# Kernel tuning notes

Hardware: AMD Instinct MI355X
Metric: run time of the kernel (lower is better)

Reference implementation:

```python
import jax, jax.numpy as jnp
import numpy as np

B, L, D = 8, 8192, 512
TARGET_RATIO = 1.0 / 6.0


def _normalize(v):
    # matches torch F.normalize(dim=-1, eps=1e-12)
    n = jnp.maximum(jnp.linalg.norm(v, axis=-1, keepdims=True), 1e-12)
    return v / n


def _downsample(x, b_hard):
    # vectorized stream compaction, padded to L (static upper bound of L_max)
    Bb, Ll, Dd = x.shape
    cnt = jnp.cumsum(b_hard.astype(jnp.int32), axis=1)
    pos = jnp.where(b_hard > 0.5, cnt - 1, Ll)          # non-selected -> dump slot L
    bidx = jnp.arange(Bb)[:, None]
    out = jnp.zeros((Bb, Ll + 1, Dd), x.dtype).at[bidx, pos].set(x)[:, :Ll]
    counts = cnt[:, -1]
    mask = jnp.arange(Ll)[None, :] < counts[:, None]
    return out, mask


def setup_inputs() -> dict:
    key = jax.random.key(0)
    k1, k2, k3 = jax.random.split(key, 3)
    x = jax.random.normal(k1, (B, L, D), jnp.float32)
    W_q = jax.random.normal(k2, (D, D), jnp.float32) / np.sqrt(D)
    W_k = jax.random.normal(k3, (D, D), jnp.float32) / np.sqrt(D)
    return {"x": x, "W_q": W_q, "W_k": W_k}


def reference(x, W_q, W_k):
    q = _normalize(jnp.einsum('bld,ed->ble', x, W_q))   # nn.Linear: x @ W.T
    k = _normalize(jnp.einsum('bld,ed->ble', x, W_k))
    k_prev = jnp.pad(k[:, :-1, :], ((0, 0), (1, 0), (0, 0)))
    cos_sim = jnp.sum(q * k_prev, axis=-1)               # (B, L)
    p = jnp.clip(0.5 * (1.0 - cos_sim), 0.0, 1.0)
    p = p.at[:, 0].set(1.0)                              # first position always boundary
    b_hard = (p >= 0.5).astype(x.dtype)
    N = 1.0 / TARGET_RATIO
    F_actual = jnp.mean(b_hard)
    G_actual = jnp.mean(p)
    ratio_loss = N / (N - 1.0) * ((N - 1.0) * F_actual * G_actual + (1.0 - F_actual) * (1.0 - G_actual))
    compressed, comp_mask = _downsample(x, b_hard)
    p_compressed, _ = _downsample(p[..., None], b_hard)
    p_compressed = p_compressed[..., 0]
    return (compressed, comp_mask, b_hard, p, p_compressed, ratio_loss)
```

## Files before the change

### kernel.cpp

```cpp
#include <hip/hip_runtime.h>
#include <hip/hip_bf16.h>
#include <math.h>

#define BB 8
#define LL 8192
#define DD 512
#define NROWS (BB * LL)

#define OUT_COMP   0
#define OUT_MASK   33554432
#define OUT_BHARD  33619968
#define OUT_P      33685504
#define OUT_PCOMP  33751040
#define OUT_LOSS   33816576

#define WS_FIXLIST 0
#define WS_FIXCNT  262144
#define WS_COUNTS  262148
#define WS_SUMP    262180
#define WS_SEL     262212
#define WS_SSK     524416
#define WS_SSQ     786560
#define WS_DOT     1048704
#define WS_WQH     1310848
#define WS_WQL     1835136
#define WS_WKH     2359424
#define WS_WKL     2883712

#define FIX_CAP 65536
#define FIX_TAU 1e-4f

typedef __attribute__((ext_vector_type(8))) _Float16 half8;
typedef __attribute__((ext_vector_type(4))) float f32x4;

static __device__ __forceinline__ void ld_g2l16(const void* g, void* l) {
  __builtin_amdgcn_global_load_lds(
      (const __attribute__((address_space(1))) void*)g,
      (__attribute__((address_space(3))) void*)l, 16, 0, 0);
}

__global__ __launch_bounds__(256) void wsplit(
    const float* __restrict__ Wq, const float* __restrict__ Wk,
    _Float16* __restrict__ wqh, _Float16* __restrict__ wql,
    _Float16* __restrict__ wkh, _Float16* __restrict__ wkl,
    float* __restrict__ ssk, float* __restrict__ ssq,
    float* __restrict__ dotb, int* __restrict__ fixcnt) {
  const int t = blockIdx.x * 256 + threadIdx.x;
  if (t == 0) *fixcnt = 0;
  ssk[t] = 0.0f;
  ssq[t] = 0.0f;
  dotb[t] = 0.0f;

  const int m = t >> 15;
  const int c = t & 32767;
  const int kt = c >> 11;
  const int ct = (c >> 6) & 31;
  const int l = c & 63;
  const int n = l & 15;
  const int kblk = l >> 4;
  const int e = ct * 16 + n;
  const int d0 = kt * 32 + kblk * 8;
  const float* src = (m ? Wk : Wq) + (long)e * 512 + d0;
  _Float16* dh = (m ? wkh : wqh) + (long)c * 8;
  _Float16* dl = (m ? wkl : wql) + (long)c * 8;
  float4 v0 = *(const float4*)src;
  float4 v1 = *(const float4*)(src + 4);
  float av[8] = {v0.x, v0.y, v0.z, v0.w, v1.x, v1.y, v1.z, v1.w};
  half8 hi, lo;
#pragma unroll
  for (int j = 0; j < 8; ++j) {
    _Float16 hh = (_Float16)av[j];
    hi[j] = hh;
    lo[j] = (_Float16)(av[j] - (float)hh);
  }
  *(half8*)dh = hi;
  *(half8*)dl = lo;
}

template <int PASS>
__global__ __launch_bounds__(256, 2) void gemm_tile(
    const float* __restrict__ x, const _Float16* __restrict__ wh,
    const _Float16* __restrict__ wl, _Float16* __restrict__ kbuf,
    float* __restrict__ ssOut, float* __restrict__ dotOut) {
  __shared__ _Float16 smem[16384];
  _Float16* AH = smem;
  _Float16* AL = AH + 4096;
  _Float16* BH = AL + 4096;
  _Float16* BL = BH + 4096;

  const int tid = threadIdx.x;
  const int lane = tid & 63;
  const int w = tid >> 6;
  const int wrow = w & 1, wcol = w >> 1;
  const int g = lane >> 4, n = lane & 15;
  const int bx = blockIdx.x;
  const int rb = bx >> 2, cb = bx & 3;
  const long r0 = (long)rb * 128;

  const int arow = ((tid >> 6) << 4) | (tid & 15);
  const int akb = (tid >> 4) & 3;
  const float* ap = x + (r0 + arow) * 512 + akb * 8;

  f32x4 acc[4][4];
#pragma unroll
  for (int mb = 0; mb < 4; ++mb)
#pragma unroll
    for (int nb = 0; nb < 4; ++nb) acc[mb][nb] = (f32x4){0.f, 0.f, 0.f, 0.f};

  float4 f0 = *(const float4*)(ap);
  float4 f1 = *(const float4*)(ap + 4);
  float4 f2 = *(const float4*)(ap + 64 * 512);
  float4 f3 = *(const float4*)(ap + 64 * 512 + 4);

  for (int kt = 0; kt < 16; ++kt) {
    const long bbase = ((long)(kt * 32 + cb * 8) << 9) + w * 1024 + lane * 8;
    ld_g2l16(wh + bbase, BH + w * 1024);
    ld_g2l16(wh + bbase + 512, BH + w * 1024 + 512);
    ld_g2l16(wl + bbase, BL + w * 1024);
    ld_g2l16(wl + bbase + 512, BL + w * 1024 + 512);
    {
      float av0[8] = {f0.x, f0.y, f0.z, f0.w, f1.x, f1.y, f1.z, f1.w};
      float av1[8] = {f2.x, f2.y, f2.z, f2.w, f3.x, f3.y, f3.z, f3.w};
      half8 h0, h1, l0, l1;
#pragma unroll
      for (int j = 0; j < 8; ++j) {
        _Float16 a = (_Float16)av0[j];
        h0[j] = a;
        l0[j] = (_Float16)(av0[j] - (float)a);
        _Float16 b = (_Float16)av1[j];
        h1[j] = b;
        l1[j] = (_Float16)(av1[j] - (float)b);
      }
      *(half8*)(AH + tid * 8) = h0;
      *(half8*)(AH + (tid + 256) * 8) = h1;
      *(half8*)(AL + tid * 8) = l0;
      *(half8*)(AL + (tid + 256) * 8) = l1;
    }
    __syncthreads();
    if (kt < 15) {
      const float* xp = ap + (kt + 1) * 32;
      f0 = *(const float4*)(xp);
      f1 = *(const float4*)(xp + 4);
      f2 = *(const float4*)(xp + 64 * 512);
      f3 = *(const float4*)(xp + 64 * 512 + 4);
    }
    half8 ah[4], al[4], bh[4], bl[4];
#pragma unroll
    for (int mb = 0; mb < 4; ++mb) {
      const int cm = wrow * 4 + mb;
      ah[mb] = *(const half8*)(AH + (cm * 64 + lane) * 8);
      al[mb] = *(const half8*)(AL + (cm * 64 + lane) * 8);
    }
#pragma unroll
    for (int nb = 0; nb < 4; ++nb) {
      bh[nb] = *(const half8*)(BH + ((wcol * 4 + nb) * 64 + lane) * 8);
      bl[nb] = *(const half8*)(BL + ((wcol * 4 + nb) * 64 + lane) * 8);
    }
#pragma unroll
    for (int nb = 0; nb < 4; ++nb)
#pragma unroll
      for (int mb = 0; mb < 4; ++mb) {
        acc[mb][nb] = __builtin_amdgcn_mfma_f32_16x16x32_f16(ah[mb], bh[nb], acc[mb][nb], 0, 0, 0);
        acc[mb][nb] = __builtin_amdgcn_mfma_f32_16x16x32_f16(al[mb], bh[nb], acc[mb][nb], 0, 0, 0);
        acc[mb][nb] = __builtin_amdgcn_mfma_f32_16x16x32_f16(ah[mb], bl[nb], acc[mb][nb], 0, 0, 0);
      }
    __syncthreads();
  }

  const int colbase = cb * 128 + wcol * 64 + n;
#pragma unroll
  for (int mb = 0; mb < 4; ++mb) {
#pragma unroll
    for (int reg = 0; reg < 4; ++reg) {
      const long row = r0 + wrow * 64 + mb * 16 + g * 4 + reg;
      float ss = 0.f, dt = 0.f;
      const long rp = (row > 0) ? row - 1 : 0;
#pragma unroll
      for (int nb = 0; nb < 4; ++nb) {
        float v = acc[mb][nb][reg];
        ss = fmaf(v, v, ss);
        if (PASS == 1) {
          kbuf[row * 512 + colbase + nb * 16] = (_Float16)v;
        } else {
          float kp = (float)kbuf[rp * 512 + colbase + nb * 16];
          dt = fmaf(v, kp, dt);
        }
      }
#pragma unroll
      for (int m = 1; m < 16; m <<= 1) {
        ss += __shfl_xor(ss, m, 64);
        if (PASS == 2) dt += __shfl_xor(dt, m, 64);
      }
      if (n == 0) {
        atomicAdd(&ssOut[row], ss);
        if (PASS == 2) atomicAdd(&dotOut[row], dt);
      }
    }
  }
}

__global__ __launch_bounds__(256) void combine(
    const float* __restrict__ ssq, const float* __restrict__ ssk,
    const float* __restrict__ dotb, float* __restrict__ dout,
    int* __restrict__ fixlist, int* __restrict__ fixcnt) {
  const int r = blockIdx.x * 256 + threadIdx.x;
  const int l = r & (LL - 1);
  float p;
  float cosv = 0.0f;
  if (l != 0) {
    float nq = fmaxf(sqrtf(ssq[r]), 1e-12f);
    float nk = fmaxf(sqrtf(ssk[r - 1]), 1e-12f);
    cosv = dotb[r] / (nq * nk);
    p = fminf(fmaxf(0.5f * (1.0f - cosv), 0.0f), 1.0f);
  } else {
    p = 1.0f;
  }
  dout[OUT_P + r] = p;
  dout[OUT_BHARD + r] = (p >= 0.5f) ? 1.0f : 0.0f;
  if (l != 0 && fabsf(cosv) < FIX_TAU) {
    int idx = atomicAdd(fixcnt, 1);
    if (idx < FIX_CAP) fixlist[idx] = r;
  }
}

__global__ __launch_bounds__(256) void fixup(
    const float* __restrict__ x, const float* __restrict__ Wq,
    const float* __restrict__ Wk, float* __restrict__ dout,
    const int* __restrict__ fixlist, const int* __restrict__ fixcnt) {
  __shared__ float xr[512], xp[512];
  __shared__ double red[3][256];
  const int t = threadIdx.x;
  int nfix = *fixcnt;
  if (nfix > FIX_CAP) nfix = FIX_CAP;

  for (int idx = blockIdx.x; idx < nfix; idx += gridDim.x) {
    const int r = fixlist[idx];
    for (int d = t; d < 512; d += 256) {
      xr[d] = x[(long)r * 512 + d];
      xp[d] = x[(long)(r - 1) * 512 + d];
    }
    __syncthreads();
    double ssq = 0.0, ssk = 0.0, dot = 0.0;
    for (int e = t; e < 512; e += 256) {
      const float* wq = Wq + (long)e * 512;
      const float* wk = Wk + (long)e * 512;
      double q = 0.0, k = 0.0;
      for (int d = 0; d < 512; ++d) {
        q = fma((double)xr[d], (double)wq[d], q);
        k = fma((double)xp[d], (double)wk[d], k);
      }
      ssq += q * q;
      ssk += k * k;
      dot += q * k;
    }
    red[0][t] = ssq;
    red[1][t] = ssk;
    red[2][t] = dot;
    __syncthreads();
    for (int s = 128; s > 0; s >>= 1) {
      if (t < s) {
        red[0][t] += red[0][t + s];
        red[1][t] += red[1][t + s];
        red[2][t] += red[2][t + s];
      }
      __syncthreads();
    }
    if (t == 0) {
      double nq = sqrt(red[0][0]);
      double nk = sqrt(red[1][0]);
      if (nq < 1e-12) nq = 1e-12;
      if (nk < 1e-12) nk = 1e-12;
      float c = (float)(red[2][0] / (nq * nk));
      float p = fminf(fmaxf(0.5f * (1.0f - c), 0.0f), 1.0f);
      dout[OUT_P + r] = p;
      dout[OUT_BHARD + r] = (p >= 0.5f) ? 1.0f : 0.0f;
    }
    __syncthreads();
  }
}

__global__ __launch_bounds__(256) void scanb(
    float* __restrict__ dout, int* __restrict__ sel,
    int* __restrict__ counts, float* __restrict__ sump) {
  __shared__ int wtot[4];
  __shared__ float wps[4];
  const int b = blockIdx.x;
  const int t = threadIdx.x;
  const int lane = t & 63, wv = t >> 6;
  const long base = (long)b * LL;

  int cnt = 0;
  float psum = 0.0f;
#pragma unroll 4
  for (int j = 0; j < 32; ++j) {
    int l = t * 32 + j;
    float bh = dout[OUT_BHARD + base + l];
    float pv = dout[OUT_P + base + l];
    cnt += (bh > 0.5f) ? 1 : 0;
    psum += pv;
  }
  int inc = cnt;
#pragma unroll
  for (int off = 1; off < 64; off <<= 1) {
    int u = __shfl_up(inc, off, 64);
    if (lane >= off) inc += u;
  }
  float ps = psum;
#pragma unroll
  for (int off = 1; off < 64; off <<= 1) ps += __shfl_xor(ps, off, 64);
  if (lane == 63) wtot[wv] = inc;
  if (lane == 0) wps[wv] = ps;
  __syncthreads();
  int wbase = 0, total = 0;
#pragma unroll
  for (int i = 0; i < 4; ++i) {
    int c = wtot[i];
    if (i < wv) wbase += c;
    total += c;
  }
  if (t == 0) {
    counts[b] = total;
    sump[b] = wps[0] + wps[1] + wps[2] + wps[3];
  }
  for (int j = 0; j < 32; ++j) {
    int l = t * 32 + j;
    dout[OUT_MASK + base + l] = (l < total) ? 1.0f : 0.0f;
    dout[OUT_PCOMP + base + l] = 0.0f;
  }
  __syncthreads();
  int pos = wbase + inc - cnt;
  for (int j = 0; j < 32; ++j) {
    int l = t * 32 + j;
    float bh = dout[OUT_BHARD + base + l];
    if (bh > 0.5f) {
      dout[OUT_PCOMP + base + pos] = dout[OUT_P + base + l];
      sel[base + pos] = l;
      ++pos;
    }
  }
}

__global__ void lossk(float* __restrict__ dout, const int* __restrict__ counts,
                      const float* __restrict__ sump) {
  if (threadIdx.x == 0 && blockIdx.x == 0) {
    float fc = 0.0f, gs = 0.0f;
    for (int b = 0; b < BB; ++b) {
      fc += (float)counts[b];
      gs += sump[b];
    }
    float F = fc / (float)NROWS;
    float G = gs / (float)NROWS;
    dout[OUT_LOSS] = 1.2f * (5.0f * F * G + (1.0f - F) * (1.0f - G));
  }
}

__global__ __launch_bounds__(128) void emit(
    const float* __restrict__ x, float* __restrict__ dout,
    const int* __restrict__ sel, const int* __restrict__ counts) {
  const long bid = blockIdx.x;
  const int b = (int)(bid >> 13);
  const int j = (int)(bid & (LL - 1));
  const int cnt = counts[b];
  float4 v = make_float4(0.0f, 0.0f, 0.0f, 0.0f);
  if (j < cnt) {
    const int l = sel[((long)b << 13) + j];
    v = *(const float4*)(x + (((long)b << 13) + l) * 512 + threadIdx.x * 4);
  }
  *(float4*)(dout + OUT_COMP + (((long)b << 13) + j) * 512 + threadIdx.x * 4) = v;
}

extern "C" void kernel_launch(void* const* d_in, const int* in_sizes, int n_in,
                              void* d_out, int out_size, void* d_ws,
                              size_t ws_size, hipStream_t stream) {
  const float* x = (const float*)d_in[0];
  const float* Wq = (const float*)d_in[1];
  const float* Wk = (const float*)d_in[2];
  float* out = (float*)d_out;
  char* ws = (char*)d_ws;

  int* fixlist = (int*)(ws + WS_FIXLIST);
  int* fixcnt = (int*)(ws + WS_FIXCNT);
  int* counts = (int*)(ws + WS_COUNTS);
  float* sump = (float*)(ws + WS_SUMP);
  int* sel = (int*)(ws + WS_SEL);
  float* ssk = (float*)(ws + WS_SSK);
  float* ssq = (float*)(ws + WS_SSQ);
  float* dotb = (float*)(ws + WS_DOT);
  _Float16* wqh = (_Float16*)(ws + WS_WQH);
  _Float16* wql = (_Float16*)(ws + WS_WQL);
  _Float16* wkh = (_Float16*)(ws + WS_WKH);
  _Float16* wkl = (_Float16*)(ws + WS_WKL);

  _Float16* kbuf = (_Float16*)(out + OUT_COMP);

  wsplit<<<256, 256, 0, stream>>>(Wq, Wk, wqh, wql, wkh, wkl, ssk, ssq, dotb, fixcnt);
  gemm_tile<1><<<2048, 256, 0, stream>>>(x, wkh, wkl, kbuf, ssk, nullptr);
  gemm_tile<2><<<2048, 256, 0, stream>>>(x, wqh, wql, kbuf, ssq, dotb);
  combine<<<NROWS / 256, 256, 0, stream>>>(ssq, ssk, dotb, out, fixlist, fixcnt);
  fixup<<<512, 256, 0, stream>>>(x, Wq, Wk, out, fixlist, fixcnt);
  scanb<<<BB, 256, 0, stream>>>(out, sel, counts, sump);
  lossk<<<1, 64, 0, stream>>>(out, counts, sump);
  emit<<<NROWS, 128, 0, stream>>>(x, out, sel, counts);
}
```

Before: 543.3 us.

## Fuse Q and K projection GEMMs into one pass with LDS-resident K tile

The two separate GEMM passes, one for K and one for Q, are merged into a single kernel. Each tile of x is now loaded and split into fp16 hi/lo parts once and multiplied against both weight matrices, with two accumulator sets. The dot product with the previous row's K is taken from a K tile staged in shared memory instead of round-tripping fp16 K through global memory. Tile-boundary rows are handled by writing edge q/k rows to scratch, and a small extra kernel computes those dots. This doubles accumulator register use and shared memory per block, which could hurt occupancy.

After: 500.9 us. 1.08x faster.

```diff
diff --git a/kernel.cpp b/kernel.cpp
--- a/kernel.cpp
+++ b/kernel.cpp
@@ -77,16 +77,20 @@
   *(half8*)dl = lo;
 }
 
-template <int PASS>
-__global__ __launch_bounds__(256, 2) void gemm_tile(
-    const float* __restrict__ x, const _Float16* __restrict__ wh,
-    const _Float16* __restrict__ wl, _Float16* __restrict__ kbuf,
-    float* __restrict__ ssOut, float* __restrict__ dotOut) {
-  __shared__ _Float16 smem[16384];
+__global__ __launch_bounds__(256, 2) void gemm_fused(
+    const float* __restrict__ x,
+    const _Float16* __restrict__ wqh, const _Float16* __restrict__ wql,
+    const _Float16* __restrict__ wkh, const _Float16* __restrict__ wkl,
+    float* __restrict__ ssqOut, float* __restrict__ sskOut,
+    float* __restrict__ dotOut,
+    float* __restrict__ qedge, float* __restrict__ kedge) {
+  __shared__ _Float16 smem[24576];
   _Float16* AH = smem;
   _Float16* AL = AH + 4096;
-  _Float16* BH = AL + 4096;
-  _Float16* BL = BH + 4096;
+  _Float16* BQH = AL + 4096;
+  _Float16* BQL = BQH + 4096;
+  _Float16* BKH = BQL + 4096;
+  _Float16* BKL = BKH + 4096;
 
   const int tid = threadIdx.x;
   const int lane = tid & 63;
@@ -101,11 +105,14 @@
   const int akb = (tid >> 4) & 3;
   const float* ap = x + (r0 + arow) * 512 + akb * 8;
 
-  f32x4 acc[4][4];
+  f32x4 accq[4][4], acck[4][4];
 #pragma unroll
   for (int mb = 0; mb < 4; ++mb)
 #pragma unroll
-    for (int nb = 0; nb < 4; ++nb) acc[mb][nb] = (f32x4){0.f, 0.f, 0.f, 0.f};
+    for (int nb = 0; nb < 4; ++nb) {
+      accq[mb][nb] = (f32x4){0.f, 0.f, 0.f, 0.f};
+      acck[mb][nb] = (f32x4){0.f, 0.f, 0.f, 0.f};
+    }
 
   float4 f0 = *(const float4*)(ap);
   float4 f1 = *(const float4*)(ap + 4);
@@ -114,10 +121,14 @@
 
   for (int kt = 0; kt < 16; ++kt) {
     const long bbase = ((long)(kt * 32 + cb * 8) << 9) + w * 1024 + lane * 8;
-    ld_g2l16(wh + bbase, BH + w * 1024);
-    ld_g2l16(wh + bbase + 512, BH + w * 1024 + 512);
-    ld_g2l16(wl + bbase, BL + w * 1024);
-    ld_g2l16(wl + bbase + 512, BL + w * 1024 + 512);
+    ld_g2l16(wqh + bbase, BQH + w * 1024);
+    ld_g2l16(wqh + bbase + 512, BQH + w * 1024 + 512);
+    ld_g2l16(wql + bbase, BQL + w * 1024);
+    ld_g2l16(wql + bbase + 512, BQL + w * 1024 + 512);
+    ld_g2l16(wkh + bbase, BKH + w * 1024);
+    ld_g2l16(wkh + bbase + 512, BKH + w * 1024 + 512);
+    ld_g2l16(wkl + bbase, BKL + w * 1024);
+    ld_g2l16(wkl + bbase + 512, BKL + w * 1024 + 512);
     {
       float av0[8] = {f0.x, f0.y, f0.z, f0.w, f1.x, f1.y, f1.z, f1.w};
       float av1[8] = {f2.x, f2.y, f2.z, f2.w, f3.x, f3.y, f3.z, f3.w};
@@ -144,59 +155,121 @@
       f2 = *(const float4*)(xp + 64 * 512);
       f3 = *(const float4*)(xp + 64 * 512 + 4);
     }
-    half8 ah[4], al[4], bh[4], bl[4];
+    half8 ah[4], al[4];
 #pragma unroll
     for (int mb = 0; mb < 4; ++mb) {
       const int cm = wrow * 4 + mb;
       ah[mb] = *(const half8*)(AH + (cm * 64 + lane) * 8);
       al[mb] = *(const half8*)(AL + (cm * 64 + lane) * 8);
     }
-#pragma unroll
-    for (int nb = 0; nb < 4; ++nb) {
-      bh[nb] = *(const half8*)(BH + ((wcol * 4 + nb) * 64 + lane) * 8);
-      bl[nb] = *(const half8*)(BL + ((wcol * 4 + nb) * 64 + lane) * 8);
-    }
+    {
+      half8 bh[4], bl[4];
+#pragma unroll
+      for (int nb = 0; nb < 4; ++nb) {
+        bh[nb] = *(const half8*)(BQH + ((wcol * 4 + nb) * 64 + lane) * 8);
+        bl[nb] = *(const half8*)(BQL + ((wcol * 4 + nb) * 64 + lane) * 8);
+      }
+#pragma unroll
+      for (int nb = 0; nb < 4; ++nb)
+#pragma unroll
+        for (int mb = 0; mb < 4; ++mb) {
+          accq[mb][nb] = __builtin_amdgcn_mfma_f32_16x16x32_f16(ah[mb], bh[nb], accq[mb][nb], 0, 0, 0);
+          accq[mb][nb] = __builtin_amdgcn_mfma_f32_16x16x32_f16(al[mb], bh[nb], accq[mb][nb], 0, 0, 0);
+          accq[mb][nb] = __builtin_amdgcn_mfma_f32_16x16x32_f16(ah[mb], bl[nb], accq[mb][nb], 0, 0, 0);
+        }
+    }
+    {
+      half8 bh[4], bl[4];
+#pragma unroll
+      for (int nb = 0; nb < 4; ++nb) {
+        bh[nb] = *(const half8*)(BKH + ((wcol * 4 + nb) * 64 + lane) * 8);
+        bl[nb] = *(const half8*)(BKL + ((wcol * 4 + nb) * 64 + lane) * 8);
+      }
+#pragma unroll
+      for (int nb = 0; nb < 4; ++nb)
+#pragma unroll
+        for (int mb = 0; mb < 4; ++mb) {
+          acck[mb][nb] = __builtin_amdgcn_mfma_f32_16x16x32_f16(ah[mb], bh[nb], acck[mb][nb], 0, 0, 0);
+          acck[mb][nb] = __builtin_amdgcn_mfma_f32_16x16x32_f16(al[mb], bh[nb], acck[mb][nb], 0, 0, 0);
+          acck[mb][nb] = __builtin_amdgcn_mfma_f32_16x16x32_f16(ah[mb], bl[nb], acck[mb][nb], 0, 0, 0);
+        }
+    }
+    __syncthreads();
+  }
+
+  _Float16* KX = smem;
+  const int col0 = wcol * 64 + n;
+  const int rbase = wrow * 64;
+#pragma unroll
+  for (int mb = 0; mb < 4; ++mb)
+#pragma unroll
+    for (int reg = 0; reg < 4; ++reg) {
+      const int rl = rbase + mb * 16 + g * 4 + reg;
+#pragma unroll
+      for (int nb = 0; nb < 4; ++nb)
+        KX[rl * 136 + col0 + nb * 16] = (_Float16)acck[mb][nb][reg];
+    }
+  __syncthreads();
+
+  if (wrow == 1 && g == 3) {
 #pragma unroll
     for (int nb = 0; nb < 4; ++nb)
-#pragma unroll
-      for (int mb = 0; mb < 4; ++mb) {
-        acc[mb][nb] = __builtin_amdgcn_mfma_f32_16x16x32_f16(ah[mb], bh[nb], acc[mb][nb], 0, 0, 0);
-        acc[mb][nb] = __builtin_amdgcn_mfma_f32_16x16x32_f16(al[mb], bh[nb], acc[mb][nb], 0, 0, 0);
-        acc[mb][nb] = __builtin_amdgcn_mfma_f32_16x16x32_f16(ah[mb], bl[nb], acc[mb][nb], 0, 0, 0);
-      }
-    __syncthreads();
-  }
-
-  const int colbase = cb * 128 + wcol * 64 + n;
+      kedge[rb * 512 + cb * 128 + col0 + nb * 16] = acck[3][nb][3];
+  }
+  if (wrow == 0 && g == 0) {
+#pragma unroll
+    for (int nb = 0; nb < 4; ++nb)
+      qedge[rb * 512 + cb * 128 + col0 + nb * 16] = accq[0][nb][0];
+  }
+
 #pragma unroll
   for (int mb = 0; mb < 4; ++mb) {
 #pragma unroll
     for (int reg = 0; reg < 4; ++reg) {
-      const long row = r0 + wrow * 64 + mb * 16 + g * 4 + reg;
-      float ss = 0.f, dt = 0.f;
-      const long rp = (row > 0) ? row - 1 : 0;
+      const int rl = rbase + mb * 16 + g * 4 + reg;
+      const long row = r0 + rl;
+      float sq = 0.f, sk = 0.f, dt = 0.f;
 #pragma unroll
       for (int nb = 0; nb < 4; ++nb) {
-        float v = acc[mb][nb][reg];
-        ss = fmaf(v, v, ss);
-        if (PASS == 1) {
-          kbuf[row * 512 + colbase + nb * 16] = (_Float16)v;
-        } else {
-          float kp = (float)kbuf[rp * 512 + colbase + nb * 16];
-          dt = fmaf(v, kp, dt);
+        float qv = accq[mb][nb][reg];
+        float kv = acck[mb][nb][reg];
+        sq = fmaf(qv, qv, sq);
+        sk = fmaf(kv, kv, sk);
+        if (rl > 0) {
+          float kp = (float)KX[(rl - 1) * 136 + col0 + nb * 16];
+          dt = fmaf(qv, kp, dt);
         }
       }
 #pragma unroll
       for (int m = 1; m < 16; m <<= 1) {
-        ss += __shfl_xor(ss, m, 64);
-        if (PASS == 2) dt += __shfl_xor(dt, m, 64);
+        sq += __shfl_xor(sq, m, 64);
+        sk += __shfl_xor(sk, m, 64);
+        dt += __shfl_xor(dt, m, 64);
       }
       if (n == 0) {
-        atomicAdd(&ssOut[row], ss);
-        if (PASS == 2) atomicAdd(&dotOut[row], dt);
-      }
-    }
-  }
+        atomicAdd(&ssqOut[row], sq);
+        atomicAdd(&sskOut[row], sk);
+        if (rl > 0) atomicAdd(&dotOut[row], dt);
+      }
+    }
+  }
+}
+
+__global__ __launch_bounds__(64) void edgedot(
+    const float* __restrict__ qedge, const float* __restrict__ kedge,
+    float* __restrict__ dotOut) {
+  const int rb = blockIdx.x;
+  if (rb == 0) return;
+  const long row = (long)rb * 128;
+  if ((row & (LL - 1)) == 0) return;
+  const int lane = threadIdx.x;
+  float dt = 0.f;
+#pragma unroll
+  for (int c = lane; c < 512; c += 64)
+    dt = fmaf(qedge[rb * 512 + c], kedge[(rb - 1) * 512 + c], dt);
+#pragma unroll
+  for (int m = 1; m < 64; m <<= 1) dt += __shfl_xor(dt, m, 64);
+  if (lane == 0) dotOut[row] = dt;
 }
 
 __global__ __launch_bounds__(256) void combine(
@@ -391,11 +464,12 @@
   _Float16* wkh = (_Float16*)(ws + WS_WKH);
   _Float16* wkl = (_Float16*)(ws + WS_WKL);
 
-  _Float16* kbuf = (_Float16*)(out + OUT_COMP);
+  float* kedge = (float*)(out + OUT_COMP);
+  float* qedge = (float*)(out + OUT_COMP + 262144);
 
   wsplit<<<256, 256, 0, stream>>>(Wq, Wk, wqh, wql, wkh, wkl, ssk, ssq, dotb, fixcnt);
-  gemm_tile<1><<<2048, 256, 0, stream>>>(x, wkh, wkl, kbuf, ssk, nullptr);
-  gemm_tile<2><<<2048, 256, 0, stream>>>(x, wqh, wql, kbuf, ssq, dotb);
+  gemm_fused<<<2048, 256, 0, stream>>>(x, wqh, wql, wkh, wkl, ssq, ssk, dotb, qedge, kedge);
+  edgedot<<<512, 64, 0, stream>>>(qedge, kedge, dotb);
   combine<<<NROWS / 256, 256, 0, stream>>>(ssq, ssk, dotb, out, fixlist, fixcnt);
   fixup<<<512, 256, 0, stream>>>(x, Wq, Wk, out, fixlist, fixcnt);
   scanb<<<BB, 256, 0, stream>>>(out, sel, counts, sump);
```
